# Optimization experiments

Measured on AMD Instinct MI355X. Metric: run time of the kernel, lower is better.

Reference implementation:

```python
import jax, jax.numpy as jnp
import numpy as np

# Sizes: B graphs of N nodes each, K nearest neighbours, D=feat_dim=nhid, C=pos_dim
B, N, K, D, C = 4, 1024, 128, 32, 2
L = 3                     # number of EGNN conv layers
E_IN = 2 * D + 1          # edge MLP input: feats_i | feats_j | rel_dist (edge_dim=0, fourier=0)
E_H = 2 * E_IN            # edge MLP hidden


def _lin(key, fan_in, fan_out):
    kw, kb = jax.random.split(key)
    w = jax.random.normal(kw, (fan_in, fan_out), jnp.float32) / np.sqrt(fan_in)
    b = jax.random.normal(kb, (fan_out,), jnp.float32) * 0.01
    return w, b


def _stack(key, fan_in, fan_out):
    ws, bs = zip(*[_lin(k, fan_in, fan_out) for k in jax.random.split(key, L)])
    return jnp.stack(ws), jnp.stack(bs)


def setup_inputs() -> dict:
    key = jax.random.key(0)
    ks = jax.random.split(key, 10)
    feat_ = jax.random.normal(ks[0], (B * N, D), jnp.float32)
    coor_ = jax.random.normal(ks[1], (B * N, C), jnp.float32)
    batch = jnp.full((B,), N, dtype=jnp.int32)   # per-graph node counts (equal-size graphs)
    embed_w, embed_b = _lin(ks[2], D, D)         # embed: Linear(feat_dim, nhid)
    e1_w, e1_b = _stack(ks[3], E_IN, E_H)        # edge MLP
    e2_w, e2_b = _stack(ks[4], E_H, D)           # -> m_dim = nhid
    gate_w, gate_b = _stack(ks[5], D, 1)         # soft_edges gate
    c1_w, c1_b = _stack(ks[6], D, 4 * D)         # coors MLP
    c2_w, c2_b = _stack(ks[7], 4 * D, 1)
    n1_w, n1_b = _stack(ks[8], 2 * D, 2 * D)     # node MLP
    n2_w, n2_b = _stack(ks[9], 2 * D, D)
    coors_scale = jnp.full((L, 1), 1e-2, jnp.float32)  # CoorsNorm scale (init 1e-2)
    return dict(feat_=feat_, coor_=coor_, batch=batch, embed_w=embed_w, embed_b=embed_b,
                e1_w=e1_w, e1_b=e1_b, e2_w=e2_w, e2_b=e2_b, gate_w=gate_w, gate_b=gate_b,
                c1_w=c1_w, c1_b=c1_b, c2_w=c2_w, c2_b=c2_b, n1_w=n1_w, n1_b=n1_b,
                n2_w=n2_w, n2_b=n2_b, coors_scale=coors_scale)


def _lrelu(x):
    return jax.nn.leaky_relu(x, 0.1)


def _gather(x, idx):
    # x: [B, n, d], idx: [B, n, k] -> [B, n, k, d]
    return jax.vmap(lambda xb, ib: xb[ib])(x, idx)


def _egnn_layer(feats, coors, p):
    (e1_w, e1_b, e2_w, e2_b, gate_w, gate_b, c1_w, c1_b, c2_w, c2_b,
     n1_w, n1_b, n2_w, n2_b, scale) = p
    # pairwise squared distances; k smallest (self included, valid_radius=inf)
    diff = coors[:, :, None, :] - coors[:, None, :, :]      # [B,n,n,C]
    dist = jnp.sum(diff * diff, axis=-1)                    # [B,n,n]
    neg_d, idx = jax.lax.top_k(-dist, K)                    # k nearest
    rel_dist = -neg_d[..., None]                            # [B,n,K,1]
    rel_coors = coors[:, :, None, :] - _gather(coors, idx)  # [B,n,K,C]
    feats_j = _gather(feats, idx)                           # [B,n,K,D]
    feats_i = jnp.broadcast_to(feats[:, :, None, :], feats_j.shape)
    edge_in = jnp.concatenate([feats_i, feats_j, rel_dist], axis=-1)  # [B,n,K,E_IN]
    # edge MLP: Lin -> act -> Lin -> act ; soft edge gate
    m = _lrelu(_lrelu(edge_in @ e1_w + e1_b) @ e2_w + e2_b)            # [B,n,K,D]
    m = m * jax.nn.sigmoid(m @ gate_w + gate_b)
    # coordinate update: coors_mlp -> scalar weights; CoorsNorm on rel coords
    cw = (_lrelu(m @ c1_w + c1_b) @ c2_w + c2_b)[..., 0]               # [B,n,K]
    norm = jnp.maximum(jnp.linalg.norm(rel_coors, axis=-1, keepdims=True), 1e-8)
    rel_n = rel_coors / norm * scale
    coors_out = jnp.einsum('bik,bikc->bic', cw, rel_n) + coors
    # feature update: sum-pool messages, node MLP with residual
    m_i = jnp.sum(m, axis=2)                                           # [B,n,D]
    node_in = jnp.concatenate([feats, m_i], axis=-1)
    feats_out = _lrelu(node_in @ n1_w + n1_b) @ n2_w + n2_b + feats
    return feats_out, coors_out


def reference(feat_, coor_, batch, embed_w, embed_b, e1_w, e1_b, e2_w, e2_b,
              gate_w, gate_b, c1_w, c1_b, c2_w, c2_b, n1_w, n1_b, n2_w, n2_b,
              coors_scale):
    # embed MLP (dropout is identity at p=0 / eval), then batch equal-size graphs
    feats = _lrelu(feat_ @ embed_w + embed_b).reshape(B, N, D)
    coors = coor_.reshape(B, N, C)
    for l in range(L):
        p = (e1_w[l], e1_b[l], e2_w[l], e2_b[l], gate_w[l], gate_b[l],
             c1_w[l], c1_b[l], c2_w[l], c2_b[l], n1_w[l], n1_b[l],
             n2_w[l], n2_b[l], coors_scale[l])
        feats, coors = _egnn_layer(feats, coors, p)
    return feats.reshape(B * N, D)
```

## Files before the change

### kernel.cpp

```cpp
#include <hip/hip_runtime.h>
#include <hip/hip_bf16.h>
#include <math.h>

#define BB 4
#define NN 1024
#define KK 128
#define DD 32
#define LL 3
#define EH 130
#define EHP 132

typedef float f32x4 __attribute__((ext_vector_type(4)));
typedef short s16x8 __attribute__((ext_vector_type(8)));

__device__ __forceinline__ float lrelu(float x) { return fmaxf(x, 0.1f * x); }

__device__ __forceinline__ unsigned pk2(float a, float b) {
    __hip_bfloat162 h = __float22bfloat162_rn(float2{a, b});
    return *(unsigned*)&h;
}
__device__ __forceinline__ unsigned short bf16_hu(float v) {
    return (unsigned short)((__float_as_uint(v) + 0x8000u) >> 16);
}
__device__ __forceinline__ unsigned short bf16_rne(float v) {
    unsigned u = __float_as_uint(v);
    return (unsigned short)((u + 0x7fffu + ((u >> 16) & 1u)) >> 16);
}

__device__ __forceinline__ void knn_select(const float2* __restrict__ cbp, int i, int lane,
                                           int* __restrict__ nb) {
    const float2 ci = cbp[i];
    unsigned k[16];
#pragma unroll
    for (int s = 0; s < 16; s++) {
        float2 cj = cbp[lane + 64 * s];
        float dx = ci.x - cj.x, dy = ci.y - cj.y;
        float d = __fadd_rn(__fmul_rn(dx, dx), __fmul_rn(dy, dy));
        k[s] = __float_as_uint(d);
    }
    unsigned P = 0;
    for (int bpos = 30; bpos >= 0; bpos--) {
        const unsigned X = P | (1u << bpos);
        unsigned c = 0;
#pragma unroll
        for (int s = 0; s < 16; s++)
            c += (unsigned)__popcll(__ballot(k[s] < X));
        if (c < (unsigned)KK) P = X;
    }
    const unsigned dstar = P;
    const unsigned long long below = (1ull << lane) - 1ull;
    unsigned run = 0;
#pragma unroll
    for (int s = 0; s < 16; s++) {
        unsigned long long m = __ballot(k[s] < dstar);
        if (k[s] < dstar) nb[run + (unsigned)__popcll(m & below)] = lane + 64 * s;
        run += (unsigned)__popcll(m);
    }
    const int need = KK - (int)run;
    unsigned tie = 0;
    for (int s = 0; s < 16 && (int)tie < need; s++) {
        unsigned long long m = __ballot(k[s] == dstar);
        if (k[s] == dstar) {
            unsigned r = tie + (unsigned)__popcll(m & below);
            if ((int)r < need) nb[run + r] = lane + 64 * s;
        }
        tie += (unsigned)__popcll(m);
    }
}

__global__ __launch_bounds__(128) void prep_kernel(
    const float* __restrict__ feat, const float* __restrict__ coor,
    const float* __restrict__ ew, const float* __restrict__ eb,
    float* __restrict__ fout,
    const float* __restrict__ e1w0, const float* __restrict__ e1b0,
    float* __restrict__ HI, float* __restrict__ HJ,
    const float* __restrict__ e2w, const float* __restrict__ e2b,
    const float* __restrict__ c1w,
    unsigned short* __restrict__ e2f, unsigned short* __restrict__ c1f) {
    const int bid = blockIdx.x;
    const int t = threadIdx.x;
    if (bid < 2048) {
        __shared__ float sfe[2][DD];
        const int n0 = bid * 2;
        if (t < 64) {
            const int nl = t >> 5, o = t & 31;
            const float* f = feat + (size_t)(n0 + nl) * DD;
            float a = eb[o];
#pragma unroll
            for (int k = 0; k < DD; k++) a = fmaf(f[k], ew[k * DD + o], a);
            a = lrelu(a);
            fout[(size_t)(n0 + nl) * DD + o] = a;
            sfe[nl][o] = a;
        }
        __syncthreads();
        for (int idx = t; idx < 2 * EHP; idx += 128) {
            const int nl = idx / EHP, o = idx - nl * EHP;
            const size_t off = (size_t)(n0 + nl) * EHP + o;
            if (o >= EH) { HI[off] = 0.f; HJ[off] = 0.f; continue; }
            const float* fl = sfe[nl];
            float aa = e1b0[o], cc = 0.f;
#pragma unroll
            for (int k = 0; k < DD; k++) aa = fmaf(fl[k], e1w0[k * EH + o], aa);
#pragma unroll
            for (int k = 0; k < DD; k++) cc = fmaf(fl[k], e1w0[(DD + k) * EH + o], cc);
            HI[off] = aa;
            HJ[off] = cc;
        }
    } else {
        const int TOT_E2 = LL * 5120;
        const int TOT = TOT_E2 + LL * 4096;
        for (int u = (bid - 2048) * 128 + t; u < TOT; u += 96 * 128) {
            if (u < TOT_E2) {
                int l = u / 5120, v = u - l * 5120;
                int jj = v & 7, la = (v >> 3) & 63, nt = (v >> 9) & 1, c = v >> 10;
                int n = nt * 16 + (la & 15);
                float val;
                if (c < 4) {
                    int k = 32 * c + (la >> 4) * 8 + jj;
                    val = e2w[(size_t)l * EH * DD + k * DD + n];
                } else {
                    int ks = (la >> 4) * 8 + jj;
                    val = (ks == 0) ? e2w[((size_t)l * EH + 128) * DD + n]
                        : (ks == 1) ? e2w[((size_t)l * EH + 129) * DD + n]
                        : (ks == 2) ? e2b[(size_t)l * DD + n] : 0.f;
                }
                e2f[u] = bf16_rne(val);
            } else {
                int v = u - TOT_E2;
                int jj = v & 7, la = (v >> 3) & 63, nt = (v >> 9) & 7, l = v >> 12;
                int k = (la >> 4) * 8 + jj;
                int n = nt * 16 + (la & 15);
                c1f[v] = bf16_rne(c1w[(size_t)l * DD * 128 + k * 128 + n]);
            }
        }
    }
}

__global__ __launch_bounds__(256) void layer_kernel(
    const float* __restrict__ feats_in, const float* __restrict__ coors_in,
    const float* __restrict__ HI, const float* __restrict__ HJ,
    const float* __restrict__ w65,
    const unsigned short* __restrict__ e2f,
    const unsigned short* __restrict__ c1f,
    const float* __restrict__ gw, const float* __restrict__ gb,
    const float* __restrict__ c1b, const float* __restrict__ c2w, const float* __restrict__ c2b,
    const float* __restrict__ n1w, const float* __restrict__ n1b,
    const float* __restrict__ n2w, const float* __restrict__ n2b,
    const float* __restrict__ scale,
    const float* __restrict__ e1wn, const float* __restrict__ e1bn,
    float* __restrict__ HIn, float* __restrict__ HJn,
    float* __restrict__ feats_out, float* __restrict__ coors_out) {
    const int node = blockIdx.x;
    const int b = node >> 10;
    const int t = threadIdx.x;
    const int lane = t & 63, wid = t >> 6;
    const int ln = lane & 15, q = lane >> 4;
    const int rowbase = wid * 32;

    __shared__ __align__(16) float shi[EHP];
    __shared__ __align__(16) float sw65[EHP];
    __shared__ __align__(16) unsigned short smA[4 * 32 * 32];
    __shared__ float sx0[128], sx1[128], su[128], sv[128], srd[128];
    __shared__ int snb[128];
    __shared__ float sgw[DD], sfi[DD], sfo[DD];
    __shared__ float sc1b[128], sc2w[128];
    __shared__ float redm[4][DD], redc[4][2];
    __shared__ float sni[2 * DD], shd[2 * DD];
    __shared__ float sp1[4][2 * DD], sp2[4][DD];

    if (t < 64) {
        knn_select((const float2*)coors_in + (size_t)b * NN, node & (NN - 1), lane, snb);
    } else {
        for (int u = t - 64; u < EHP; u += 192) {
            shi[u] = HI[(size_t)node * EHP + u];
            sw65[u] = (u < EH) ? w65[u] : 0.f;
        }
        if (t - 64 < DD) { sfi[t - 64] = feats_in[node * DD + (t - 64)]; sgw[t - 64] = gw[t - 64]; }
        if (t >= 128) { sc1b[t - 128] = c1b[t - 128]; sc2w[t - 128] = c2w[t - 128]; }
    }
    __syncthreads();

    const float cix = coors_in[node * 2], ciy = coors_in[node * 2 + 1];
    if (t < 128) {
        const int j = snb[t];
        const float2 cj = *(const float2*)(coors_in + ((size_t)(b * NN) + j) * 2);
        const float dx = cix - cj.x, dy = ciy - cj.y;
        const float rd = __fadd_rn(__fmul_rn(dx, dx), __fmul_rn(dy, dy));
        srd[t] = rd;
        const float nrm = fmaxf(sqrtf(rd), 1e-8f);
        const float s = scale[0] / nrm;
        su[t] = dx * s;
        sv[t] = dy * s;
        const float2 hjt = *(const float2*)(HJ + ((size_t)(b * NN) + j) * EHP + 128);
        sx0[t] = lrelu(shi[128] + hjt.x + rd * sw65[128]);
        sx1[t] = lrelu(shi[129] + hjt.y + rd * sw65[129]);
    }
    __syncthreads();

    float rdR[2];
    const float* hjb[2];
#pragma unroll
    for (int mt = 0; mt < 2; mt++) {
        const int row = rowbase + mt * 16 + ln;
        rdR[mt] = srd[row];
        hjb[mt] = HJ + ((size_t)(b * NN) + snb[row]) * EHP;
    }

    const float4* shi4 = (const float4*)shi;
    const float4* sw4  = (const float4*)sw65;

    const f32x4 zz = {0.f, 0.f, 0.f, 0.f};
    f32x4 accA[2][2];
    accA[0][0] = zz; accA[0][1] = zz; accA[1][0] = zz; accA[1][1] = zz;

    float4 ha[2], hbv[2];
#pragma unroll
    for (int mt = 0; mt < 2; mt++) {
        const float4* hjp = (const float4*)(hjb[mt] + q * 8);
        ha[mt] = hjp[0];
        hbv[mt] = hjp[1];
    }
    s16x8 bcur0 = *(const s16x8*)(e2f + (0 * 64 + lane) * 8);
    s16x8 bcur1 = *(const s16x8*)(e2f + (1 * 64 + lane) * 8);

#pragma unroll 1
    for (int c = 0; c < 4; c++) {
        s16x8 bn0 = *(const s16x8*)(e2f + (((c + 1) * 2 + 0) * 64 + lane) * 8);
        s16x8 bn1 = *(const s16x8*)(e2f + (((c + 1) * 2 + 1) * 64 + lane) * 8);
        float4 nha[2], nhb[2];
        if (c < 3) {
#pragma unroll
            for (int mt = 0; mt < 2; mt++) {
                const float4* hjp = (const float4*)(hjb[mt] + (c + 1) * 32 + q * 8);
                nha[mt] = hjp[0];
                nhb[mt] = hjp[1];
            }
        }
        const int kb = c * 8 + q * 2;
        const float4 hi0 = shi4[kb], hi1 = shi4[kb + 1];
        const float4 wv0 = sw4[kb],  wv1 = sw4[kb + 1];
#pragma unroll
        for (int mt = 0; mt < 2; mt++) {
            const float r = rdR[mt];
            union { s16x8 v; unsigned u[4]; } A;
            A.u[0] = pk2(lrelu(hi0.x + ha[mt].x + r * wv0.x), lrelu(hi0.y + ha[mt].y + r * wv0.y));
            A.u[1] = pk2(lrelu(hi0.z + ha[mt].z + r * wv0.z), lrelu(hi0.w + ha[mt].w + r * wv0.w));
            A.u[2] = pk2(lrelu(hi1.x + hbv[mt].x + r * wv1.x), lrelu(hi1.y + hbv[mt].y + r * wv1.y));
            A.u[3] = pk2(lrelu(hi1.z + hbv[mt].z + r * wv1.z), lrelu(hi1.w + hbv[mt].w + r * wv1.w));
            accA[mt][0] = __builtin_amdgcn_mfma_f32_16x16x32_bf16(A.v, bcur0, accA[mt][0], 0, 0, 0);
            accA[mt][1] = __builtin_amdgcn_mfma_f32_16x16x32_bf16(A.v, bcur1, accA[mt][1], 0, 0, 0);
        }
#pragma unroll
        for (int mt = 0; mt < 2; mt++) { ha[mt] = nha[mt]; hbv[mt] = nhb[mt]; }
        bcur0 = bn0; bcur1 = bn1;
    }

    {
#pragma unroll
        for (int mt = 0; mt < 2; mt++) {
            const int row = rowbase + mt * 16 + ln;
            union { s16x8 v; unsigned u[4]; } A;
            const unsigned p0 = pk2(sx0[row], sx1[row]);
            A.u[0] = (q == 0) ? p0 : 0u;
            A.u[1] = (q == 0) ? 0x00003f80u : 0u;
            A.u[2] = 0u;
            A.u[3] = 0u;
            accA[mt][0] = __builtin_amdgcn_mfma_f32_16x16x32_bf16(A.v, bcur0, accA[mt][0], 0, 0, 0);
            accA[mt][1] = __builtin_amdgcn_mfma_f32_16x16x32_bf16(A.v, bcur1, accA[mt][1], 0, 0, 0);
        }
    }

    s16x8 cfr[8];
#pragma unroll
    for (int g8 = 0; g8 < 8; g8++)
        cfr[g8] = *(const s16x8*)(c1f + (g8 * 64 + lane) * 8);

#pragma unroll
    for (int mt = 0; mt < 2; mt++)
#pragma unroll
        for (int nt = 0; nt < 2; nt++)
#pragma unroll
            for (int r = 0; r < 4; r++)
                accA[mt][nt][r] = lrelu(accA[mt][nt][r]);

    const float gbv = gb[0];
#pragma unroll
    for (int mt = 0; mt < 2; mt++) {
        float p[4];
#pragma unroll
        for (int r = 0; r < 4; r++)
            p[r] = accA[mt][0][r] * sgw[ln] + accA[mt][1][r] * sgw[16 + ln];
#pragma unroll
        for (int off = 1; off <= 8; off <<= 1)
#pragma unroll
            for (int r = 0; r < 4; r++) p[r] += __shfl_xor(p[r], off);
#pragma unroll
        for (int r = 0; r < 4; r++) {
            const float g = 1.f / (1.f + __expf(-(p[r] + gbv)));
            accA[mt][0][r] *= g;
            accA[mt][1][r] *= g;
        }
    }

    float mi0 = 0.f, mi1 = 0.f;
#pragma unroll
    for (int mt = 0; mt < 2; mt++)
#pragma unroll
        for (int r = 0; r < 4; r++) { mi0 += accA[mt][0][r]; mi1 += accA[mt][1][r]; }
    mi0 += __shfl_xor(mi0, 16); mi0 += __shfl_xor(mi0, 32);
    mi1 += __shfl_xor(mi1, 16); mi1 += __shfl_xor(mi1, 32);
    if (lane < 16) { redm[wid][lane] = mi0; redm[wid][16 + lane] = mi1; }

    unsigned short* smw = smA + wid * (32 * 32);
#pragma unroll
    for (int mt = 0; mt < 2; mt++)
#pragma unroll
        for (int nt = 0; nt < 2; nt++)
#pragma unroll
            for (int r = 0; r < 4; r++) {
                const int prow = (r << 3) | (4 * mt + q);
                smw[prow * 32 + nt * 16 + ln] = bf16_hu(accA[mt][nt][r]);
            }

    s16x8 a4[2];
#pragma unroll
    for (int mt = 0; mt < 2; mt++) {
        const int prow = ((ln & 3) << 3) | (4 * mt + (ln >> 2));
        a4[mt] = *(const s16x8*)(smw + prow * 32 + q * 8);
    }

    float cacc[2][4];
#pragma unroll
    for (int mt = 0; mt < 2; mt++)
#pragma unroll
        for (int r = 0; r < 4; r++) cacc[mt][r] = 0.f;

#pragma unroll
    for (int g = 0; g < 4; g++) {
        const float cb0 = sc1b[(2 * g + 0) * 16 + ln];
        const float cb1 = sc1b[(2 * g + 1) * 16 + ln];
        const f32x4 ci0 = {cb0, cb0, cb0, cb0};
        const f32x4 ci1 = {cb1, cb1, cb1, cb1};
        f32x4 c20[2], c21[2];
#pragma unroll
        for (int mt = 0; mt < 2; mt++) {
            c20[mt] = __builtin_amdgcn_mfma_f32_16x16x32_bf16(a4[mt], cfr[2 * g + 0], ci0, 0, 0, 0);
            c21[mt] = __builtin_amdgcn_mfma_f32_16x16x32_bf16(a4[mt], cfr[2 * g + 1], ci1, 0, 0, 0);
        }
#pragma unroll
        for (int h = 0; h < 2; h++) {
            const float c2wv = sc2w[(2 * g + h) * 16 + ln];
#pragma unroll
            for (int mt = 0; mt < 2; mt++)
#pragma unroll
                for (int r = 0; r < 4; r++) {
                    const float v = (h ? c21[mt][r] : c20[mt][r]);
                    cacc[mt][r] = fmaf(lrelu(v), c2wv, cacc[mt][r]);
                }
        }
    }
#pragma unroll
    for (int off = 1; off <= 8; off <<= 1)
#pragma unroll
        for (int mt = 0; mt < 2; mt++)
#pragma unroll
            for (int r = 0; r < 4; r++) cacc[mt][r] += __shfl_xor(cacc[mt][r], off);

    const float c2bv = c2b[0];
    float vxp = 0.f, vyp = 0.f;
    if (ln == 0) {
#pragma unroll
        for (int mt = 0; mt < 2; mt++)
#pragma unroll
            for (int r = 0; r < 4; r++) {
                const int row = rowbase + mt * 16 + q * 4 + r;
                const float cw = cacc[mt][r] + c2bv;
                vxp = fmaf(cw, su[row], vxp);
                vyp = fmaf(cw, sv[row], vyp);
            }
    }
    vxp += __shfl_xor(vxp, 16); vxp += __shfl_xor(vxp, 32);
    vyp += __shfl_xor(vyp, 16); vyp += __shfl_xor(vyp, 32);
    if (lane == 0) { redc[wid][0] = vxp; redc[wid][1] = vyp; }

    __syncthreads();
    if (t < DD) {
        sni[t] = sfi[t];
        sni[DD + t] = redm[0][t] + redm[1][t] + redm[2][t] + redm[3][t];
    }
    __syncthreads();
    {
        const int o = t & 63, p = t >> 6;
        float a = 0.f;
#pragma unroll
        for (int k = 0; k < 16; k++) a = fmaf(sni[p * 16 + k], n1w[(p * 16 + k) * 64 + o], a);
        sp1[p][o] = a;
    }
    __syncthreads();
    if (t < 2 * DD)
        shd[t] = lrelu(n1b[t] + ((sp1[0][t] + sp1[1][t]) + (sp1[2][t] + sp1[3][t])));
    __syncthreads();
    if (t < 128) {
        const int o = t & 31, p = t >> 5;
        float a = 0.f;
#pragma unroll
        for (int k = 0; k < 16; k++) a = fmaf(shd[p * 16 + k], n2w[(p * 16 + k) * DD + o], a);
        sp2[p][o] = a;
    }
    __syncthreads();
    if (t < DD) {
        const float val = n2b[t] + ((sp2[0][t] + sp2[1][t]) + (sp2[2][t] + sp2[3][t])) + sfi[t];
        feats_out[node * DD + t] = val;
        sfo[t] = val;
    }
    if (t == 0) {
        coors_out[node * 2]     = cix + redc[0][0] + redc[1][0] + redc[2][0] + redc[3][0];
        coors_out[node * 2 + 1] = ciy + redc[0][1] + redc[1][1] + redc[2][1] + redc[3][1];
    }
    __syncthreads();

    if (e1wn) {
        for (int idx = t; idx < 2 * EHP; idx += 256) {
            const int nl = idx / EHP, o = idx - nl * EHP;
            float* dst = (nl ? HJn : HIn) + (size_t)node * EHP + o;
            if (o >= EH) { *dst = 0.f; continue; }
            const int rowoff = nl ? DD : 0;
            float a = nl ? 0.f : e1bn[o];
#pragma unroll
            for (int k = 0; k < DD; k++) a = fmaf(sfo[k], e1wn[(rowoff + k) * EH + o], a);
            *dst = a;
        }
    }
}

extern "C" void kernel_launch(void* const* d_in, const int* in_sizes, int n_in,
                              void* d_out, int out_size, void* d_ws, size_t ws_size,
                              hipStream_t stream) {
    const float* feat_   = (const float*)d_in[0];
    const float* coor_   = (const float*)d_in[1];
    const float* embed_w = (const float*)d_in[3];
    const float* embed_b = (const float*)d_in[4];
    const float* e1_w    = (const float*)d_in[5];
    const float* e1_b    = (const float*)d_in[6];
    const float* e2_w    = (const float*)d_in[7];
    const float* e2_b    = (const float*)d_in[8];
    const float* gate_w  = (const float*)d_in[9];
    const float* gate_b  = (const float*)d_in[10];
    const float* c1_w    = (const float*)d_in[11];
    const float* c1_b    = (const float*)d_in[12];
    const float* c2_w    = (const float*)d_in[13];
    const float* c2_b    = (const float*)d_in[14];
    const float* n1_w    = (const float*)d_in[15];
    const float* n1_b    = (const float*)d_in[16];
    const float* n2_w    = (const float*)d_in[17];
    const float* n2_b    = (const float*)d_in[18];
    const float* cscale  = (const float*)d_in[19];

    float* ws = (float*)d_ws;
    float* fa   = ws;   ws += BB * NN * DD;
    float* fb   = ws;   ws += BB * NN * DD;
    float* ca   = ws;   ws += BB * NN * 2;
    float* cb2  = ws;   ws += BB * NN * 2;
    float* HI0  = ws;   ws += BB * NN * EHP;
    float* HJ0  = ws;   ws += BB * NN * EHP;
    float* HI1  = ws;   ws += BB * NN * EHP;
    float* HJ1  = ws;   ws += BB * NN * EHP;
    unsigned short* e2f = (unsigned short*)ws;
    unsigned short* c1f = e2f + LL * 5120;

    prep_kernel<<<2048 + 96, 128, 0, stream>>>(feat_, coor_, embed_w, embed_b, fa,
                                               e1_w, e1_b, HI0, HJ0,
                                               e2_w, e2_b, c1_w, e2f, c1f);

    float* HIbuf[2] = {HI0, HI1};
    float* HJbuf[2] = {HJ0, HJ1};
    const float* fin = fa;
    const float* cin = coor_;
    float* fouts[LL] = {fb, fa, (float*)d_out};
    float* couts[LL] = {ca, cb2, ca};

    for (int l = 0; l < LL; l++) {
        const int cur = l & 1, nxt = (l + 1) & 1;
        layer_kernel<<<BB * NN, 256, 0, stream>>>(
            fin, cin, HIbuf[cur], HJbuf[cur],
            e1_w + ((size_t)l * 65 + 64) * EH,
            e2f + (size_t)l * 5120,
            c1f + (size_t)l * 4096,
            gate_w + (size_t)l * DD,
            gate_b + l,
            c1_b + (size_t)l * 128,
            c2_w + (size_t)l * 128,
            c2_b + l,
            n1_w + (size_t)l * 64 * 64,
            n1_b + (size_t)l * 64,
            n2_w + (size_t)l * 64 * 32,
            n2_b + (size_t)l * DD,
            cscale + l,
            (l < LL - 1) ? (e1_w + (size_t)(l + 1) * 65 * EH) : nullptr,
            (l < LL - 1) ? (e1_b + (size_t)(l + 1) * EH) : nullptr,
            HIbuf[nxt], HJbuf[nxt],
            fouts[l], couts[l]);
        fin = fouts[l];
        cin = couts[l];
    }
}
```

Before: 334.7 us.

## Replace bitwise kNN threshold search with 4-pass radix histogram select

The k-th smallest distance threshold in the kNN selection is now found with a four-pass 8-bit radix select, using an LDS histogram built with shared atomics and a wave prefix scan, instead of 31 bitwise binary-search iterations of ballot/popcount over 16 registers. The histogram reuses the smA shared buffer, so a __syncthreads is added before smA is later written with message data. The unused coor argument is also dropped from prep_kernel. The change cuts the number of ballot rounds but adds LDS atomics, which contend when many keys share a bin, plus one extra block barrier.

```diff
diff --git a/kernel.cpp b/kernel.cpp
--- a/kernel.cpp
+++ b/kernel.cpp
@@ -28,6 +28,7 @@
 }
 
 __device__ __forceinline__ void knn_select(const float2* __restrict__ cbp, int i, int lane,
+                                           unsigned* __restrict__ hist,
                                            int* __restrict__ nb) {
     const float2 ci = cbp[i];
     unsigned k[16];
@@ -38,16 +39,52 @@
         float d = __fadd_rn(__fmul_rn(dx, dx), __fmul_rn(dy, dy));
         k[s] = __float_as_uint(d);
     }
-    unsigned P = 0;
-    for (int bpos = 30; bpos >= 0; bpos--) {
-        const unsigned X = P | (1u << bpos);
-        unsigned c = 0;
-#pragma unroll
-        for (int s = 0; s < 16; s++)
-            c += (unsigned)__popcll(__ballot(k[s] < X));
-        if (c < (unsigned)KK) P = X;
-    }
-    const unsigned dstar = P;
+    unsigned prefix = 0u;
+    unsigned r = KK - 1;
+#pragma unroll
+    for (int pass = 0; pass < 4; pass++) {
+        const int sh = 24 - 8 * pass;
+        const unsigned mpref = (pass == 0) ? 0u : (0xFFFFFFFFu << (sh + 8));
+        ((uint4*)hist)[lane] = uint4{0u, 0u, 0u, 0u};
+        __threadfence_block();
+#pragma unroll
+        for (int s = 0; s < 16; s++) {
+            if ((k[s] & mpref) == prefix)
+                atomicAdd(&hist[(k[s] >> sh) & 255u], 1u);
+        }
+        __threadfence_block();
+        const uint4 h = ((const uint4*)hist)[lane];
+        const unsigned partial = h.x + h.y + h.z + h.w;
+        unsigned incl = partial;
+#pragma unroll
+        for (int off = 1; off < 64; off <<= 1) {
+            unsigned v = __shfl_up(incl, off, 64);
+            if (lane >= off) incl += v;
+        }
+        const unsigned excl = incl - partial;
+        const bool own = (r >= excl) && (r < incl);
+        unsigned enc = 0u;
+        if (own) {
+            unsigned hh[4] = {h.x, h.y, h.z, h.w};
+            unsigned e = excl;
+            int bin = -1;
+#pragma unroll
+            for (int ii = 0; ii < 4; ii++) {
+                if (bin < 0) {
+                    if (r < e + hh[ii]) bin = ii;
+                    else e += hh[ii];
+                }
+            }
+            enc = (((unsigned)(4 * lane + bin)) << 16) | (r - e);
+        }
+        const unsigned long long mk = __ballot(own);
+        const int src = __ffsll((unsigned long long)mk) - 1;
+        enc = __shfl(enc, src, 64);
+        prefix |= (enc >> 16) << sh;
+        r = enc & 0xFFFFu;
+    }
+    const unsigned dstar = prefix;
+
     const unsigned long long below = (1ull << lane) - 1ull;
     unsigned run = 0;
 #pragma unroll
@@ -61,15 +98,15 @@
     for (int s = 0; s < 16 && (int)tie < need; s++) {
         unsigned long long m = __ballot(k[s] == dstar);
         if (k[s] == dstar) {
-            unsigned r = tie + (unsigned)__popcll(m & below);
-            if ((int)r < need) nb[run + r] = lane + 64 * s;
+            unsigned r2 = tie + (unsigned)__popcll(m & below);
+            if ((int)r2 < need) nb[run + r2] = lane + 64 * s;
         }
         tie += (unsigned)__popcll(m);
     }
 }
 
 __global__ __launch_bounds__(128) void prep_kernel(
-    const float* __restrict__ feat, const float* __restrict__ coor,
+    const float* __restrict__ feat,
     const float* __restrict__ ew, const float* __restrict__ eb,
     float* __restrict__ fout,
     const float* __restrict__ e1w0, const float* __restrict__ e1b0,
@@ -169,7 +206,8 @@
     __shared__ float sp1[4][2 * DD], sp2[4][DD];
 
     if (t < 64) {
-        knn_select((const float2*)coors_in + (size_t)b * NN, node & (NN - 1), lane, snb);
+        knn_select((const float2*)coors_in + (size_t)b * NN, node & (NN - 1), lane,
+                   (unsigned*)smA, snb);
     } else {
         for (int u = t - 64; u < EHP; u += 192) {
             shi[u] = HI[(size_t)node * EHP + u];
@@ -311,6 +349,7 @@
     mi1 += __shfl_xor(mi1, 16); mi1 += __shfl_xor(mi1, 32);
     if (lane < 16) { redm[wid][lane] = mi0; redm[wid][16 + lane] = mi1; }
 
+    __syncthreads();
     unsigned short* smw = smA + wid * (32 * 32);
 #pragma unroll
     for (int mt = 0; mt < 2; mt++)
@@ -468,7 +507,7 @@
     unsigned short* e2f = (unsigned short*)ws;
     unsigned short* c1f = e2f + LL * 5120;
 
-    prep_kernel<<<2048 + 96, 128, 0, stream>>>(feat_, coor_, embed_w, embed_b, fa,
+    prep_kernel<<<2048 + 96, 128, 0, stream>>>(feat_, embed_w, embed_b, fa,
                                                e1_w, e1_b, HI0, HJ0,
                                                e2_w, e2_b, c1_w, e2f, c1f);
 
```

Measured after the change: 328.7 us. No clear change (-1.8%).
